# Kernel optimization log

Measured on AMD Instinct MI355X. Metric: run time of the kernel, lower is better.

## Reference

```python
import jax, jax.numpy as jnp
import numpy as np
import math

DT_SCALE = 1.0
DT_MIN, DT_MAX = 0.001, 0.1


def setup_inputs() -> dict:
    key = jax.random.key(0)
    ku, kdt, ka, kb, kc = jax.random.split(key, 5)
    batch, seq_len, d_model, d_state = 32, 4096, 256, 64
    u = jax.random.normal(ku, (batch, seq_len, d_model), dtype=jnp.float32)
    # log_dt ~ U[log(dt_min), log(dt_max)]
    log_dt = jax.random.uniform(kdt, (d_model,), dtype=jnp.float32) * (
        math.log(DT_MAX) - math.log(DT_MIN)) + math.log(DT_MIN)
    # A_real = -exp(U(-1, 1))  (strictly negative -> stable recurrence)
    A_real = -jnp.exp(jax.random.uniform(ka, (d_model, d_state), dtype=jnp.float32) * 2.0 - 1.0)
    B = jax.random.normal(kb, (d_model, d_state), dtype=jnp.float32)
    C = jax.random.normal(kc, (d_model, d_state), dtype=jnp.float32)
    x0 = jnp.zeros((d_model, d_state), dtype=jnp.float32)
    return {"u": u, "log_dt": log_dt, "A_real": A_real, "B": B, "C": C, "x0": x0}


def reference(u, log_dt, A_real, B, C, x0):
    # u: (batch, seq_len, d_model)
    batch = u.shape[0]
    dt = jnp.exp(log_dt) * DT_SCALE                      # (D,)
    A_tilde = jnp.exp(A_real * dt[:, None])              # (D, N)
    B_tilde = (1.0 - A_tilde) * B / A_real               # (D, N)
    x_init = jnp.broadcast_to(x0, (batch,) + x0.shape)   # (B, D, N)

    def step(x, u_t):
        # x: (B, D, N), u_t: (B, D)
        x = A_tilde * x + B_tilde * u_t[..., None]
        y = jnp.sum(C * x, axis=-1)                      # (B, D)
        return x, y

    u_t_major = jnp.swapaxes(u, 0, 1)                    # (L, B, D)
    _, ys = jax.lax.scan(step, x_init, u_t_major)        # ys: (L, B, D)
    return jnp.swapaxes(ys, 0, 1)                        # (B, L, D)
```

## Files before the change

kernel.cpp:

```cpp
#include <hip/hip_runtime.h>
#include <math.h>

#define BATCH 32
#define SEQ   4096
#define DM    256
#define NS    64


__device__ __forceinline__ void load_a(const float* __restrict__ log_dt,
                                       const float* __restrict__ A_real,
                                       int d, int n0, float* a) {
    float dt = expf(log_dt[d]);
    const float* Ap = A_real + d * NS + n0;
#pragma unroll
    for (int k = 0; k < 16; ++k)
        a[k] = expf(Ap[k] * dt);
}

__global__ __launch_bounds__(256, 8)
void pass1_kernel(const float* __restrict__ u,
                  const float* __restrict__ log_dt,
                  const float* __restrict__ A_real,
                  float* __restrict__ S, int Tc) {
    int wave = (blockIdx.x * blockDim.x + threadIdx.x) >> 6;
    int lane = threadIdx.x & 63;
    int wc = wave & 511;
    int g  = wave >> 9;
    int b  = wc >> 4;
    int d0 = (wc & 15) << 4;
    int c   = lane >> 2;
    int sub = lane & 3;
    int d   = d0 + c;
    int n0  = sub << 4;

    float a[16], z[16];
    load_a(log_dt, A_real, d, n0, a);
#pragma unroll
    for (int k = 0; k < 16; ++k) z[k] = 0.0f;

    int t0 = g * Tc;
    int tl = lane >> 4;
    const float* ubase = u + (size_t)b * SEQ * DM + d0 + (lane & 15);

    float ucur = ubase[(size_t)(t0 + tl) * DM];
    for (int t4 = 0; t4 < Tc; t4 += 4) {
        int tn = (t4 + 4 < Tc) ? (t0 + t4 + 4 + tl) : (t0 + tl);
        float unext = ubase[(size_t)tn * DM];
#pragma unroll
        for (int s = 0; s < 4; ++s) {
            float uv = __shfl(ucur, (s << 4) + c);
#pragma unroll
            for (int k = 0; k < 16; ++k)
                z[k] = fmaf(a[k], z[k], uv);
        }
        ucur = unext;
    }

    float* Sp = S + (((size_t)g * BATCH + b) * DM + d) * NS + n0;
    float4* Sp4 = (float4*)Sp;
#pragma unroll
    for (int j = 0; j < 4; ++j)
        Sp4[j] = make_float4(z[4 * j], z[4 * j + 1], z[4 * j + 2], z[4 * j + 3]);
}

__global__ void pass2_kernel(float* __restrict__ S,
                             const float* __restrict__ log_dt,
                             const float* __restrict__ A_real,
                             const float* __restrict__ B,
                             const float* __restrict__ x0,
                             int C, int Tc) {
    int idx = blockIdx.x * blockDim.x + threadIdx.x;
    if (idx >= BATCH * DM * NS) return;
    int dn = idx & (DM * NS - 1);
    int d = dn >> 6;
    float ar = A_real[dn];
    float dt = expf(log_dt[d]);
    float aT = expf(ar * dt * (float)Tc);
    float x0v = x0[dn];
    float prev;
    if (x0v == 0.0f) {
        prev = 0.0f;
    } else {
        float at = expf(ar * dt);
        float bt = (1.0f - at) * B[dn] / ar;
        prev = (bt != 0.0f) ? (x0v / bt) : 0.0f;
    }
    for (int g = 0; g < C; ++g) {
        float* p = S + (size_t)g * (BATCH * DM * NS) + idx;
        float s = *p;
        *p = prev;
        prev = fmaf(aT, prev, s);
    }
}

__global__ __launch_bounds__(256, 6)
void pass3_kernel(const float* __restrict__ u,
                  const float* __restrict__ log_dt,
                  const float* __restrict__ A_real,
                  const float* __restrict__ B,
                  const float* __restrict__ Cm,
                  const float* __restrict__ S,
                  const float* __restrict__ x0,
                  float* __restrict__ y, int Tc, int useS) {
    int wave = (blockIdx.x * blockDim.x + threadIdx.x) >> 6;
    int lane = threadIdx.x & 63;
    int wc = wave & 511;
    int g  = wave >> 9;
    int b  = wc >> 4;
    int d0 = (wc & 15) << 4;
    int c   = lane >> 2;
    int sub = lane & 3;
    int d   = d0 + c;
    int n0  = sub << 4;

    float a[16], cbt[16], z[16];
    {
        float dt = expf(log_dt[d]);
        const float* Ap = A_real + d * NS + n0;
        const float* Bp = B + d * NS + n0;
        const float* Cp = Cm + d * NS + n0;
#pragma unroll
        for (int k = 0; k < 16; ++k) {
            float ar = Ap[k];
            float at = expf(ar * dt);
            a[k] = at;
            cbt[k] = Cp[k] * ((1.0f - at) * Bp[k] / ar);
        }
        if (useS) {
            const float4* Sp4 = (const float4*)(S +
                (((size_t)g * BATCH + b) * DM + d) * NS + n0);
#pragma unroll
            for (int j = 0; j < 4; ++j) {
                float4 v = Sp4[j];
                z[4 * j] = v.x; z[4 * j + 1] = v.y;
                z[4 * j + 2] = v.z; z[4 * j + 3] = v.w;
            }
        } else {
            const float* Xp = x0 + d * NS + n0;
            const float* Bp2 = B + d * NS + n0;
#pragma unroll
            for (int k = 0; k < 16; ++k) {
                float x0v = Xp[k];
                if (x0v == 0.0f) { z[k] = 0.0f; }
                else {
                    float bt = (1.0f - a[k]) * Bp2[k] / (A_real + d * NS + n0)[k];
                    z[k] = (bt != 0.0f) ? (x0v / bt) : 0.0f;
                }
            }
        }
    }

    int t0 = g * Tc;
    int tl = lane >> 4;
    const float* ubase = u + (size_t)b * SEQ * DM + d0 + (lane & 15);
    float* ybase = y + (size_t)b * SEQ * DM + d;

    float ucur = ubase[(size_t)(t0 + tl) * DM];
    for (int t4 = 0; t4 < Tc; t4 += 4) {
        int tn = (t4 + 4 < Tc) ? (t0 + t4 + 4 + tl) : (t0 + tl);
        float unext = ubase[(size_t)tn * DM];
#pragma unroll
        for (int s = 0; s < 4; ++s) {
            float uv = __shfl(ucur, (s << 4) + c);
            float p0 = 0.0f, p1 = 0.0f;
#pragma unroll
            for (int k = 0; k < 16; k += 2) {
                z[k] = fmaf(a[k], z[k], uv);
                p0 = fmaf(cbt[k], z[k], p0);
                z[k + 1] = fmaf(a[k + 1], z[k + 1], uv);
                p1 = fmaf(cbt[k + 1], z[k + 1], p1);
            }
            float p = p0 + p1;
            p += __shfl_xor(p, 1);
            p += __shfl_xor(p, 2);
            if (sub == 0)
                ybase[(size_t)(t0 + t4 + s) * DM] = p;
        }
        ucur = unext;
    }
}

extern "C" void kernel_launch(void* const* d_in, const int* in_sizes, int n_in,
                              void* d_out, int out_size, void* d_ws, size_t ws_size,
                              hipStream_t stream) {
    const float* u      = (const float*)d_in[0];
    const float* log_dt = (const float*)d_in[1];
    const float* A_real = (const float*)d_in[2];
    const float* B      = (const float*)d_in[3];
    const float* Cm     = (const float*)d_in[4];
    const float* x0     = (const float*)d_in[5];
    float* y = (float*)d_out;
    float* S = (float*)d_ws;

    const size_t per_chunk = (size_t)BATCH * DM * NS * sizeof(float);
    int C = 16;
    while (C > 1 && (size_t)C * per_chunk > ws_size) C >>= 1;
    if ((size_t)C * per_chunk > ws_size) C = 1;
    int Tc = SEQ / C;

    if (C > 1) {
        pass1_kernel<<<dim3(C * 128), dim3(256), 0, stream>>>(
            u, log_dt, A_real, S, Tc);
        pass2_kernel<<<dim3((BATCH * DM * NS) / 256), dim3(256), 0, stream>>>(
            S, log_dt, A_real, B, x0, C, Tc);
    }
    pass3_kernel<<<dim3(C * 128), dim3(256), 0, stream>>>(
        u, log_dt, A_real, B, Cm, S, x0, y, Tc, (C > 1) ? 1 : 0);
}
```

Before: 429.8 us.

## Give each lane 32 states and drop shuffle-based u broadcast, use 32 chunks

Each thread now owns 32 of the 64 state entries for one channel (two lanes per channel instead of four), so each lane loads its u value straight from global memory. This removes the per-step shuffle broadcast and one of the two reduction shuffles. The chunk count goes from 16 to 32 to keep the same number of waves, which doubles the workspace traffic in the serial pass2 sweep. Register use per thread rises, so launch bounds drop to 4 blocks per SM; the per-step global u loads are now redundant across lane pairs.

Measured after the change: 590.5 us. +37.4%, slower.

```diff
diff --git a/kernel.cpp b/kernel.cpp
--- a/kernel.cpp
+++ b/kernel.cpp
@@ -7,59 +7,53 @@
 #define NS    64
 
 
-__device__ __forceinline__ void load_a(const float* __restrict__ log_dt,
-                                       const float* __restrict__ A_real,
-                                       int d, int n0, float* a) {
-    float dt = expf(log_dt[d]);
-    const float* Ap = A_real + d * NS + n0;
-#pragma unroll
-    for (int k = 0; k < 16; ++k)
-        a[k] = expf(Ap[k] * dt);
-}
-
-__global__ __launch_bounds__(256, 8)
+__global__ __launch_bounds__(256, 4)
 void pass1_kernel(const float* __restrict__ u,
                   const float* __restrict__ log_dt,
                   const float* __restrict__ A_real,
                   float* __restrict__ S, int Tc) {
     int wave = (blockIdx.x * blockDim.x + threadIdx.x) >> 6;
     int lane = threadIdx.x & 63;
-    int wc = wave & 511;
-    int g  = wave >> 9;
-    int b  = wc >> 4;
-    int d0 = (wc & 15) << 4;
-    int c   = lane >> 2;
-    int sub = lane & 3;
+    int wc = wave & 255;
+    int g  = wave >> 8;
+    int b  = wc >> 3;
+    int d0 = (wc & 7) << 5;
+    int c   = lane >> 1;
+    int sub = lane & 1;
     int d   = d0 + c;
-    int n0  = sub << 4;
-
-    float a[16], z[16];
-    load_a(log_dt, A_real, d, n0, a);
-#pragma unroll
-    for (int k = 0; k < 16; ++k) z[k] = 0.0f;
+    int n0  = sub << 5;
+
+    float a[32], z[32];
+    {
+        float dt = expf(log_dt[d]);
+        const float* Ap = A_real + d * NS + n0;
+#pragma unroll
+        for (int k = 0; k < 32; ++k) {
+            a[k] = expf(Ap[k] * dt);
+            z[k] = 0.0f;
+        }
+    }
 
     int t0 = g * Tc;
-    int tl = lane >> 4;
-    const float* ubase = u + (size_t)b * SEQ * DM + d0 + (lane & 15);
-
-    float ucur = ubase[(size_t)(t0 + tl) * DM];
-    for (int t4 = 0; t4 < Tc; t4 += 4) {
-        int tn = (t4 + 4 < Tc) ? (t0 + t4 + 4 + tl) : (t0 + tl);
-        float unext = ubase[(size_t)tn * DM];
-#pragma unroll
-        for (int s = 0; s < 4; ++s) {
-            float uv = __shfl(ucur, (s << 4) + c);
-#pragma unroll
-            for (int k = 0; k < 16; ++k)
-                z[k] = fmaf(a[k], z[k], uv);
-        }
+    const float* uptr = u + (size_t)b * SEQ * DM + (size_t)t0 * DM + d;
+
+    float ucur = *uptr;
+    for (int t = 0; t < Tc - 1; ++t) {
+        float unext = uptr[DM];
+        uptr += DM;
+#pragma unroll
+        for (int k = 0; k < 32; ++k)
+            z[k] = fmaf(a[k], z[k], ucur);
         ucur = unext;
     }
+#pragma unroll
+    for (int k = 0; k < 32; ++k)
+        z[k] = fmaf(a[k], z[k], ucur);
 
     float* Sp = S + (((size_t)g * BATCH + b) * DM + d) * NS + n0;
     float4* Sp4 = (float4*)Sp;
 #pragma unroll
-    for (int j = 0; j < 4; ++j)
+    for (int j = 0; j < 8; ++j)
         Sp4[j] = make_float4(z[4 * j], z[4 * j + 1], z[4 * j + 2], z[4 * j + 3]);
 }
 
@@ -93,7 +87,7 @@
     }
 }
 
-__global__ __launch_bounds__(256, 6)
+__global__ __launch_bounds__(256, 4)
 void pass3_kernel(const float* __restrict__ u,
                   const float* __restrict__ log_dt,
                   const float* __restrict__ A_real,
@@ -104,23 +98,23 @@
                   float* __restrict__ y, int Tc, int useS) {
     int wave = (blockIdx.x * blockDim.x + threadIdx.x) >> 6;
     int lane = threadIdx.x & 63;
-    int wc = wave & 511;
-    int g  = wave >> 9;
-    int b  = wc >> 4;
-    int d0 = (wc & 15) << 4;
-    int c   = lane >> 2;
-    int sub = lane & 3;
+    int wc = wave & 255;
+    int g  = wave >> 8;
+    int b  = wc >> 3;
+    int d0 = (wc & 7) << 5;
+    int c   = lane >> 1;
+    int sub = lane & 1;
     int d   = d0 + c;
-    int n0  = sub << 4;
-
-    float a[16], cbt[16], z[16];
+    int n0  = sub << 5;
+
+    float a[32], cbt[32], z[32];
     {
         float dt = expf(log_dt[d]);
         const float* Ap = A_real + d * NS + n0;
         const float* Bp = B + d * NS + n0;
         const float* Cp = Cm + d * NS + n0;
 #pragma unroll
-        for (int k = 0; k < 16; ++k) {
+        for (int k = 0; k < 32; ++k) {
             float ar = Ap[k];
             float at = expf(ar * dt);
             a[k] = at;
@@ -130,20 +124,19 @@
             const float4* Sp4 = (const float4*)(S +
                 (((size_t)g * BATCH + b) * DM + d) * NS + n0);
 #pragma unroll
-            for (int j = 0; j < 4; ++j) {
+            for (int j = 0; j < 8; ++j) {
                 float4 v = Sp4[j];
                 z[4 * j] = v.x; z[4 * j + 1] = v.y;
                 z[4 * j + 2] = v.z; z[4 * j + 3] = v.w;
             }
         } else {
             const float* Xp = x0 + d * NS + n0;
-            const float* Bp2 = B + d * NS + n0;
-#pragma unroll
-            for (int k = 0; k < 16; ++k) {
+#pragma unroll
+            for (int k = 0; k < 32; ++k) {
                 float x0v = Xp[k];
                 if (x0v == 0.0f) { z[k] = 0.0f; }
                 else {
-                    float bt = (1.0f - a[k]) * Bp2[k] / (A_real + d * NS + n0)[k];
+                    float bt = (1.0f - a[k]) * Bp[k] / Ap[k];
                     z[k] = (bt != 0.0f) ? (x0v / bt) : 0.0f;
                 }
             }
@@ -151,32 +144,39 @@
     }
 
     int t0 = g * Tc;
-    int tl = lane >> 4;
-    const float* ubase = u + (size_t)b * SEQ * DM + d0 + (lane & 15);
-    float* ybase = y + (size_t)b * SEQ * DM + d;
-
-    float ucur = ubase[(size_t)(t0 + tl) * DM];
-    for (int t4 = 0; t4 < Tc; t4 += 4) {
-        int tn = (t4 + 4 < Tc) ? (t0 + t4 + 4 + tl) : (t0 + tl);
-        float unext = ubase[(size_t)tn * DM];
-#pragma unroll
-        for (int s = 0; s < 4; ++s) {
-            float uv = __shfl(ucur, (s << 4) + c);
-            float p0 = 0.0f, p1 = 0.0f;
-#pragma unroll
-            for (int k = 0; k < 16; k += 2) {
-                z[k] = fmaf(a[k], z[k], uv);
-                p0 = fmaf(cbt[k], z[k], p0);
-                z[k + 1] = fmaf(a[k + 1], z[k + 1], uv);
-                p1 = fmaf(cbt[k + 1], z[k + 1], p1);
-            }
-            float p = p0 + p1;
-            p += __shfl_xor(p, 1);
-            p += __shfl_xor(p, 2);
-            if (sub == 0)
-                ybase[(size_t)(t0 + t4 + s) * DM] = p;
-        }
+    const float* uptr = u + (size_t)b * SEQ * DM + (size_t)t0 * DM + d;
+    float* yptr = y + (size_t)b * SEQ * DM + (size_t)t0 * DM + d;
+
+    float ucur = *uptr;
+    for (int t = 0; t < Tc - 1; ++t) {
+        float unext = uptr[DM];
+        uptr += DM;
+        float p0 = 0.0f, p1 = 0.0f, p2 = 0.0f, p3 = 0.0f;
+#pragma unroll
+        for (int k = 0; k < 32; k += 4) {
+            z[k]     = fmaf(a[k],     z[k],     ucur); p0 = fmaf(cbt[k],     z[k],     p0);
+            z[k + 1] = fmaf(a[k + 1], z[k + 1], ucur); p1 = fmaf(cbt[k + 1], z[k + 1], p1);
+            z[k + 2] = fmaf(a[k + 2], z[k + 2], ucur); p2 = fmaf(cbt[k + 2], z[k + 2], p2);
+            z[k + 3] = fmaf(a[k + 3], z[k + 3], ucur); p3 = fmaf(cbt[k + 3], z[k + 3], p3);
+        }
+        float p = (p0 + p1) + (p2 + p3);
+        p += __shfl_xor(p, 1);
+        if (sub == 0) *yptr = p;
+        yptr += DM;
         ucur = unext;
+    }
+    {
+        float p0 = 0.0f, p1 = 0.0f, p2 = 0.0f, p3 = 0.0f;
+#pragma unroll
+        for (int k = 0; k < 32; k += 4) {
+            z[k]     = fmaf(a[k],     z[k],     ucur); p0 = fmaf(cbt[k],     z[k],     p0);
+            z[k + 1] = fmaf(a[k + 1], z[k + 1], ucur); p1 = fmaf(cbt[k + 1], z[k + 1], p1);
+            z[k + 2] = fmaf(a[k + 2], z[k + 2], ucur); p2 = fmaf(cbt[k + 2], z[k + 2], p2);
+            z[k + 3] = fmaf(a[k + 3], z[k + 3], ucur); p3 = fmaf(cbt[k + 3], z[k + 3], p3);
+        }
+        float p = (p0 + p1) + (p2 + p3);
+        p += __shfl_xor(p, 1);
+        if (sub == 0) *yptr = p;
     }
 }
 
@@ -193,17 +193,17 @@
     float* S = (float*)d_ws;
 
     const size_t per_chunk = (size_t)BATCH * DM * NS * sizeof(float);
-    int C = 16;
+    int C = 32;
     while (C > 1 && (size_t)C * per_chunk > ws_size) C >>= 1;
     if ((size_t)C * per_chunk > ws_size) C = 1;
     int Tc = SEQ / C;
 
     if (C > 1) {
-        pass1_kernel<<<dim3(C * 128), dim3(256), 0, stream>>>(
+        pass1_kernel<<<dim3(C * 64), dim3(256), 0, stream>>>(
             u, log_dt, A_real, S, Tc);
         pass2_kernel<<<dim3((BATCH * DM * NS) / 256), dim3(256), 0, stream>>>(
             S, log_dt, A_real, B, x0, C, Tc);
     }
-    pass3_kernel<<<dim3(C * 128), dim3(256), 0, stream>>>(
+    pass3_kernel<<<dim3(C * 64), dim3(256), 0, stream>>>(
         u, log_dt, A_real, B, Cm, S, x0, y, Tc, (C > 1) ? 1 : 0);
 }
```
